# Optimization experiments

Hardware: AMD Instinct MI355X
Metric: run time of the kernel (lower is better)

Reference implementation:

```python
import jax, jax.numpy as jnp
import numpy as np

B, HDIM, H, W = 1, 256, 48, 48
KDIM = 2048
TOP = int(0.1 * KDIM)  # 204, matches int(0.1*self.k)


def _l2norm(v):
    # matches torch F.normalize(dim=1, eps=1e-12)
    return v / jnp.maximum(jnp.linalg.norm(v, axis=1, keepdims=True), 1e-12)


def setup_inputs() -> dict:
    key = jax.random.key(0)
    k1, k2, k3 = jax.random.split(key, 3)
    return {
        "x": jax.random.normal(k1, (B, HDIM, H, W), dtype=jnp.float32),
        "feat_units": jax.random.normal(k2, (KDIM, HDIM), dtype=jnp.float32),
        "label_units": jax.random.normal(k3, (KDIM, 4), dtype=jnp.float32),
    }


def reference(x, feat_units, label_units):
    # update_flag='topk', y=None path of MemoryN2N.forward
    b, c, h, w = x.shape
    xf = x.transpose(0, 2, 3, 1).reshape(-1, c)          # (n, c)
    score = _l2norm(xf) @ _l2norm(feat_units).T           # (n, k) cosine scores
    weight = jax.nn.softmax(score, axis=1)                # (n, k)
    # torch.sort(descending)[1][:, :TOP] == top_k indices (same values)
    _, top_idx = jax.lax.top_k(score, TOP)                # (n, TOP) int32
    sel_wt = jnp.take_along_axis(weight, top_idx, axis=1)  # (n, TOP)
    out_x = jnp.einsum('nk,nkc->nc', sel_wt, feat_units[top_idx])   # (n, c)
    out_y = jnp.einsum('nk,nkc->nc', sel_wt, label_units[top_idx])  # (n, 4)

    def to_img(t, ch):
        return t.reshape(b, h, w, ch).transpose(0, 3, 1, 2)

    out = jnp.concatenate([x, to_img(out_x, c), to_img(out_y, 4)], axis=1)  # (b, 2c+4, h, w)
    return out, score
```

## Files before the change

kernel.cpp:

```cpp
#include <hip/hip_runtime.h>
#include <math.h>

#define N_PIX 2304
#define CDIM  256
#define KDIM  2048
#define TOPK  204

typedef __attribute__((ext_vector_type(8))) short bf16x8;
typedef __attribute__((ext_vector_type(4))) float f32x4;

__device__ __forceinline__ unsigned short f2bf(float f) {
    unsigned u = __float_as_uint(f);
    unsigned r = u + 0x7FFFu + ((u >> 16) & 1u);
    return (unsigned short)(r >> 16);
}
__device__ __forceinline__ float bf2f(unsigned short h) {
    return __uint_as_float((unsigned)h << 16);
}

__device__ __forceinline__ void gload16(const void* g, void* l) {
    __builtin_amdgcn_global_load_lds((const __attribute__((address_space(1))) void*)g,
                                     (__attribute__((address_space(3))) void*)l,
                                     16, 0, 0);
}

__global__ __launch_bounds__(256) void k_prep(const float* __restrict__ x,
                                              const float* __restrict__ feat,
                                              const float* __restrict__ label,
                                              float* __restrict__ out,
                                              unsigned short* __restrict__ xn,
                                              unsigned short* __restrict__ fnorm,
                                              unsigned short* __restrict__ F2T) {
    __shared__ __align__(16) char sm[36864];
    int b = blockIdx.x, t = threadIdx.x;

    if (b < 36) {
        unsigned short* tile = (unsigned short*)sm;
        float* part  = (float*)(sm + 34816);
        float* rnloc = (float*)(sm + 35840);
        int p0 = b * 64;
        #pragma unroll
        for (int i = 0; i < 16; ++i) {
            int g  = i * 256 + t;
            int c  = g >> 4;
            int p4 = g & 15;
            float4 v = *(const float4*)(x + (size_t)c * N_PIX + p0 + p4 * 4);
            *(float4*)(out + (size_t)c * N_PIX + p0 + p4 * 4) = v;
            ushort4 pk;
            pk.x = f2bf(v.x); pk.y = f2bf(v.y); pk.z = f2bf(v.z); pk.w = f2bf(v.w);
            *(ushort4*)&tile[c * 68 + p4 * 4] = pk;
        }
        __syncthreads();
        {
            int pixel = t & 63, q = t >> 6;
            float s = 0.f;
            #pragma unroll
            for (int i = 0; i < 64; ++i) {
                float v = bf2f(tile[(q * 64 + i) * 68 + pixel]);
                s = fmaf(v, v, s);
            }
            part[q * 64 + pixel] = s;
        }
        __syncthreads();
        if (t < 64) {
            float tt = part[t] + part[64 + t] + part[128 + t] + part[192 + t];
            rnloc[t] = 1.0f / fmaxf(sqrtf(tt), 1e-12f);
        }
        __syncthreads();
        {
            int p = t >> 2, cq = t & 3;
            float rn = rnloc[p];
            #pragma unroll
            for (int j = 0; j < 8; ++j) {
                bf16x8 pk;
                #pragma unroll
                for (int jj = 0; jj < 8; ++jj)
                    pk[jj] = (short)f2bf(bf2f(tile[(cq * 64 + j * 8 + jj) * 68 + p]) * rn);
                *(bf16x8*)(xn + (size_t)(p0 + p) * CDIM + cq * 64 + j * 8) = pk;
            }
        }
    } else {
        unsigned short* tile = (unsigned short*)sm;
        int r0 = (b - 36) * 64;
        #pragma unroll
        for (int i = 0; i < 16; ++i) {
            int g  = i * 256 + t;
            int r  = g >> 6;
            int c4 = g & 63;
            float4 v = *(const float4*)(feat + (size_t)(r0 + r) * CDIM + c4 * 4);
            ushort4 pk;
            pk.x = f2bf(v.x); pk.y = f2bf(v.y); pk.z = f2bf(v.z); pk.w = f2bf(v.w);
            *(ushort4*)&tile[r * 264 + c4 * 4] = pk;
        }
        __syncthreads();
        int row = t >> 2, q = t & 3;
        float s = 0.f;
        #pragma unroll
        for (int i = 0; i < 64; ++i) {
            float v = bf2f(tile[row * 264 + q * 64 + i]);
            s = fmaf(v, v, s);
        }
        s += __shfl_xor(s, 1, 64);
        s += __shfl_xor(s, 2, 64);
        float rn = 1.0f / fmaxf(sqrtf(s), 1e-12f);
        #pragma unroll
        for (int j = 0; j < 8; ++j) {
            bf16x8 pk;
            #pragma unroll
            for (int jj = 0; jj < 8; ++jj)
                pk[jj] = (short)f2bf(bf2f(tile[row * 264 + q * 64 + j * 8 + jj]) * rn);
            *(bf16x8*)(fnorm + (size_t)(r0 + row) * CDIM + q * 64 + j * 8) = pk;
        }
        __syncthreads();
        {
            int rp = (t & 31) * 2, cg2 = t >> 5;
            #pragma unroll
            for (int i = 0; i < 32; ++i) {
                int c = i * 8 + cg2;
                unsigned u0 = tile[rp * 264 + c];
                unsigned u1 = tile[(rp + 1) * 264 + c];
                *(unsigned*)(F2T + (size_t)c * KDIM + r0 + rp) = u0 | (u1 << 16);
            }
        }
        {
            int ch = t >> 6, r = t & 63;
            F2T[(size_t)(256 + ch) * KDIM + r0 + r] = f2bf(label[(size_t)(r0 + r) * 4 + ch]);
        }
        #pragma unroll
        for (int i = 0; i < 15; ++i) {
            int idx = t + i * 256;
            int zr = idx >> 6, zc = idx & 63;
            F2T[(size_t)(260 + zr) * KDIM + r0 + zc] = 0;
        }
    }
}

__global__ __launch_bounds__(256) void k_gemm1(const unsigned short* __restrict__ A,
                                               const unsigned short* __restrict__ B,
                                               float* __restrict__ C) {
    __shared__ __align__(16) unsigned short smA[2][128 * 32];
    __shared__ __align__(16) unsigned short smB[2][128 * 32];
    int t = threadIdx.x, l = t & 63, w = t >> 6;
    int m0 = blockIdx.y * 128, n0 = blockIdx.x * 128;
    int wr = w >> 1, wc = w & 1;

    f32x4 acc[4][4] = {};

    #pragma unroll
    for (int r = 0; r < 2; ++r) {
        int row = r * 64 + w * 16 + (l >> 2);
        int ch  = (l & 3) ^ ((row >> 1) & 3);
        gload16(A + (size_t)(m0 + row) * CDIM + ch * 8, &smA[0][(r * 64 + w * 16) * 32]);
        gload16(B + (size_t)(n0 + row) * CDIM + ch * 8, &smB[0][(r * 64 + w * 16) * 32]);
    }
    __syncthreads();

    for (int ks = 0; ks < 8; ++ks) {
        int cur = ks & 1;
        if (ks < 7) {
            int k0 = (ks + 1) * 32;
            #pragma unroll
            for (int r = 0; r < 2; ++r) {
                int row = r * 64 + w * 16 + (l >> 2);
                int ch  = (l & 3) ^ ((row >> 1) & 3);
                gload16(A + (size_t)(m0 + row) * CDIM + k0 + ch * 8, &smA[cur ^ 1][(r * 64 + w * 16) * 32]);
                gload16(B + (size_t)(n0 + row) * CDIM + k0 + ch * 8, &smB[cur ^ 1][(r * 64 + w * 16) * 32]);
            }
        }
        bf16x8 av[4], bv[4];
        #pragma unroll
        for (int mi = 0; mi < 4; ++mi) {
            int R = wr * 64 + mi * 16 + (l & 15);
            av[mi] = *(const bf16x8*)&smA[cur][R * 32 + (((l >> 4) ^ ((R >> 1) & 3)) << 3)];
        }
        #pragma unroll
        for (int ni = 0; ni < 4; ++ni) {
            int R = wc * 64 + ni * 16 + (l & 15);
            bv[ni] = *(const bf16x8*)&smB[cur][R * 32 + (((l >> 4) ^ ((R >> 1) & 3)) << 3)];
        }
        #pragma unroll
        for (int mi = 0; mi < 4; ++mi)
            #pragma unroll
            for (int ni = 0; ni < 4; ++ni)
                acc[mi][ni] = __builtin_amdgcn_mfma_f32_16x16x32_bf16(av[mi], bv[ni], acc[mi][ni], 0, 0, 0);
        __syncthreads();
    }

    #pragma unroll
    for (int mi = 0; mi < 4; ++mi)
        #pragma unroll
        for (int ni = 0; ni < 4; ++ni) {
            int rbase = m0 + wr * 64 + mi * 16 + (l >> 4) * 4;
            int cidx  = n0 + wc * 64 + ni * 16 + (l & 15);
            #pragma unroll
            for (int r = 0; r < 4; ++r)
                C[(size_t)(rbase + r) * KDIM + cidx] = acc[mi][ni][r];
        }
}

__global__ __launch_bounds__(256) void k_select(const float* __restrict__ score,
                                                unsigned short* __restrict__ Wm) {
    int t = threadIdx.x, l = t & 63, w = t >> 6;
    int row = blockIdx.x * 4 + w;
    const float* srow = score + (size_t)row * KDIM;

    float s[32];
    #pragma unroll
    for (int j = 0; j < 8; ++j) {
        float4 v = *(const float4*)(srow + j * 256 + l * 4);
        s[j * 4 + 0] = v.x; s[j * 4 + 1] = v.y; s[j * 4 + 2] = v.z; s[j * 4 + 3] = v.w;
    }

    float d = 0.f;
    #pragma unroll
    for (int j = 0; j < 32; ++j) d += __expf(s[j]);
    #pragma unroll
    for (int off = 32; off; off >>= 1) d += __shfl_xor(d, off, 64);
    float rd = 1.0f / d;

    float lo = -0.25f, hi = 0.75f;
    #pragma unroll 1
    for (int it = 0; it < 18; ++it) {
        float mid = 0.5f * (lo + hi);
        int c = 0;
        #pragma unroll
        for (int j = 0; j < 32; ++j)
            c += (int)__popcll(__ballot(s[j] > mid));
        if (c >= TOPK) lo = mid; else hi = mid;
    }

    #pragma unroll
    for (int j = 0; j < 8; ++j) {
        ushort4 pk;
        pk.x = (s[j*4+0] > lo) ? f2bf(__expf(s[j*4+0]) * rd) : (unsigned short)0;
        pk.y = (s[j*4+1] > lo) ? f2bf(__expf(s[j*4+1]) * rd) : (unsigned short)0;
        pk.z = (s[j*4+2] > lo) ? f2bf(__expf(s[j*4+2]) * rd) : (unsigned short)0;
        pk.w = (s[j*4+3] > lo) ? f2bf(__expf(s[j*4+3]) * rd) : (unsigned short)0;
        *(ushort4*)(Wm + (size_t)row * KDIM + j * 256 + l * 4) = pk;
    }
}

__global__ __launch_bounds__(256) void k_gemm2(const unsigned short* __restrict__ W,
                                               const unsigned short* __restrict__ F2T,
                                               float* __restrict__ out) {
    __shared__ __align__(16) char sm[65536];
    int t = threadIdx.x, l = t & 63, w = t >> 6;
    int m0 = blockIdx.y * 64, n0 = blockIdx.x * 64;
    char* wbase = sm + w * 16384;
    int   kb    = w * 512;

    f32x4 acc[4][4] = {};

    #pragma unroll
    for (int i = 0; i < 4; ++i) {
        int row = i * 16 + (l >> 2);
        int ch  = (l & 3) ^ ((row >> 1) & 3);
        gload16(W   + (size_t)(m0 + row) * KDIM + kb + ch * 8, wbase + i * 1024);
        gload16(F2T + (size_t)(n0 + row) * KDIM + kb + ch * 8, wbase + 8192 + i * 1024);
    }

    for (int ks = 0; ks < 16; ++ks) {
        int cur = ks & 1;
        if (ks < 15) {
            int koff = kb + (ks + 1) * 32;
            #pragma unroll
            for (int i = 0; i < 4; ++i) {
                int row = i * 16 + (l >> 2);
                int ch  = (l & 3) ^ ((row >> 1) & 3);
                gload16(W   + (size_t)(m0 + row) * KDIM + koff + ch * 8, wbase + (cur ^ 1) * 4096 + i * 1024);
                gload16(F2T + (size_t)(n0 + row) * KDIM + koff + ch * 8, wbase + 8192 + (cur ^ 1) * 4096 + i * 1024);
            }
            asm volatile("s_waitcnt vmcnt(8)" ::: "memory");
        } else {
            asm volatile("s_waitcnt vmcnt(0)" ::: "memory");
        }
        bf16x8 av[4], bv[4];
        #pragma unroll
        for (int mi = 0; mi < 4; ++mi) {
            int R = mi * 16 + (l & 15);
            av[mi] = *(const bf16x8*)(wbase + cur * 4096 + R * 64 + (((l >> 4) ^ ((R >> 1) & 3)) << 4));
        }
        #pragma unroll
        for (int ni = 0; ni < 4; ++ni) {
            int R = ni * 16 + (l & 15);
            bv[ni] = *(const bf16x8*)(wbase + 8192 + cur * 4096 + R * 64 + (((l >> 4) ^ ((R >> 1) & 3)) << 4));
        }
        #pragma unroll
        for (int mi = 0; mi < 4; ++mi)
            #pragma unroll
            for (int ni = 0; ni < 4; ++ni)
                acc[mi][ni] = __builtin_amdgcn_mfma_f32_16x16x32_bf16(av[mi], bv[ni], acc[mi][ni], 0, 0, 0);
    }

    __syncthreads();
    float* tl = (float*)sm;
    if (w >= 2) {
        float* dst = tl + (w - 2) * 64 * 65;
        #pragma unroll
        for (int mi = 0; mi < 4; ++mi)
            #pragma unroll
            for (int ni = 0; ni < 4; ++ni) {
                int rr = mi * 16 + (l >> 4) * 4;
                int cc = ni * 16 + (l & 15);
                #pragma unroll
                for (int r = 0; r < 4; ++r)
                    dst[(rr + r) * 65 + cc] = acc[mi][ni][r];
            }
    }
    __syncthreads();
    if (w < 2) {
        float* dst = tl + w * 64 * 65;
        #pragma unroll
        for (int mi = 0; mi < 4; ++mi)
            #pragma unroll
            for (int ni = 0; ni < 4; ++ni) {
                int rr = mi * 16 + (l >> 4) * 4;
                int cc = ni * 16 + (l & 15);
                #pragma unroll
                for (int r = 0; r < 4; ++r)
                    dst[(rr + r) * 65 + cc] += acc[mi][ni][r];
            }
    }
    __syncthreads();
    int pl = t & 63, cg2 = t >> 6;
    #pragma unroll
    for (int i = 0; i < 16; ++i) {
        int cc = cg2 * 16 + i;
        int c_out = n0 + cc;
        int orow;
        if (c_out < 256) orow = 256 + c_out;
        else if (c_out < 260) orow = 512 + (c_out - 256);
        else continue;
        out[(size_t)orow * N_PIX + m0 + pl] = tl[pl * 65 + cc] + tl[64 * 65 + pl * 65 + cc];
    }
}

extern "C" void kernel_launch(void* const* d_in, const int* in_sizes, int n_in,
                              void* d_out, int out_size, void* d_ws, size_t ws_size,
                              hipStream_t stream) {
    const float* x     = (const float*)d_in[0];
    const float* feat  = (const float*)d_in[1];
    const float* label = (const float*)d_in[2];
    float* out   = (float*)d_out;
    float* score = out + 516 * N_PIX;

    char* ws = (char*)d_ws;
    unsigned short* xn    = (unsigned short*)(ws);
    unsigned short* fnorm = (unsigned short*)(ws + 1179648);
    unsigned short* F2T   = (unsigned short*)(ws + 2228224);
    unsigned short* Wm    = (unsigned short*)(ws + 3538944);

    k_prep  <<<68,           256, 0, stream>>>(x, feat, label, out, xn, fnorm, F2T);
    k_gemm1 <<<dim3(16, 18), 256, 0, stream>>>(xn, fnorm, score);
    k_select<<<576,          256, 0, stream>>>(score, Wm);
    k_gemm2 <<<dim3(5, 36),  256, 0, stream>>>(Wm, F2T, out);
}
```

Measured before the change: 52.37 us.

## Shrink prep and gemm1 tiles for more blocks; threshold on exp values in select

The prep kernel now handles 16 pixels or 16 feature rows per block instead of 64, which quadruples the grid to 272 blocks and reworks the per-thread reduction and transpose mappings. gemm1 uses 64-row M tiles, doubling its grid to 576 blocks so more of the GPU's compute units are occupied. The select kernel computes exp once, reuses it for the softmax denominator, the threshold bisection (bounds moved into exp space) and the output, which removes the repeated exp calls. In exchange, operand reuse per block drops in gemm1 and more blocks and launches add overhead.

```diff
diff --git a/kernel.cpp b/kernel.cpp
--- a/kernel.cpp
+++ b/kernel.cpp
@@ -31,59 +31,62 @@
                                               unsigned short* __restrict__ xn,
                                               unsigned short* __restrict__ fnorm,
                                               unsigned short* __restrict__ F2T) {
-    __shared__ __align__(16) char sm[36864];
+    __shared__ __align__(16) char sm[12288];
     int b = blockIdx.x, t = threadIdx.x;
 
-    if (b < 36) {
+    if (b < 144) {
         unsigned short* tile = (unsigned short*)sm;
-        float* part  = (float*)(sm + 34816);
-        float* rnloc = (float*)(sm + 35840);
-        int p0 = b * 64;
-        #pragma unroll
-        for (int i = 0; i < 16; ++i) {
+        float* part  = (float*)(sm + 10240);
+        float* rnloc = (float*)(sm + 11264);
+        int p0 = b * 16;
+        #pragma unroll
+        for (int i = 0; i < 4; ++i) {
             int g  = i * 256 + t;
-            int c  = g >> 4;
-            int p4 = g & 15;
+            int c  = g >> 2;
+            int p4 = g & 3;
             float4 v = *(const float4*)(x + (size_t)c * N_PIX + p0 + p4 * 4);
             *(float4*)(out + (size_t)c * N_PIX + p0 + p4 * 4) = v;
             ushort4 pk;
             pk.x = f2bf(v.x); pk.y = f2bf(v.y); pk.z = f2bf(v.z); pk.w = f2bf(v.w);
-            *(ushort4*)&tile[c * 68 + p4 * 4] = pk;
+            *(ushort4*)&tile[c * 20 + p4 * 4] = pk;
         }
         __syncthreads();
         {
-            int pixel = t & 63, q = t >> 6;
+            int px = t & 15, cg = t >> 4;
             float s = 0.f;
             #pragma unroll
-            for (int i = 0; i < 64; ++i) {
-                float v = bf2f(tile[(q * 64 + i) * 68 + pixel]);
+            for (int i = 0; i < 16; ++i) {
+                float v = bf2f(tile[(cg * 16 + i) * 20 + px]);
                 s = fmaf(v, v, s);
             }
-            part[q * 64 + pixel] = s;
-        }
-        __syncthreads();
-        if (t < 64) {
-            float tt = part[t] + part[64 + t] + part[128 + t] + part[192 + t];
+            part[cg * 16 + px] = s;
+        }
+        __syncthreads();
+        if (t < 16) {
+            float tt = 0.f;
+            #pragma unroll
+            for (int cg = 0; cg < 16; ++cg) tt += part[cg * 16 + t];
             rnloc[t] = 1.0f / fmaxf(sqrtf(tt), 1e-12f);
         }
         __syncthreads();
         {
-            int p = t >> 2, cq = t & 3;
-            float rn = rnloc[p];
-            #pragma unroll
-            for (int j = 0; j < 8; ++j) {
+            int px = t >> 4;
+            float rn = rnloc[px];
+            #pragma unroll
+            for (int ji = 0; ji < 2; ++ji) {
+                int j = (t & 15) + ji * 16;
                 bf16x8 pk;
                 #pragma unroll
                 for (int jj = 0; jj < 8; ++jj)
-                    pk[jj] = (short)f2bf(bf2f(tile[(cq * 64 + j * 8 + jj) * 68 + p]) * rn);
-                *(bf16x8*)(xn + (size_t)(p0 + p) * CDIM + cq * 64 + j * 8) = pk;
+                    pk[jj] = (short)f2bf(bf2f(tile[(j * 8 + jj) * 20 + px]) * rn);
+                *(bf16x8*)(xn + (size_t)(p0 + px) * CDIM + j * 8) = pk;
             }
         }
     } else {
         unsigned short* tile = (unsigned short*)sm;
-        int r0 = (b - 36) * 64;
-        #pragma unroll
-        for (int i = 0; i < 16; ++i) {
+        int r0 = (b - 144) * 16;
+        #pragma unroll
+        for (int i = 0; i < 4; ++i) {
             int g  = i * 256 + t;
             int r  = g >> 6;
             int c4 = g & 63;
@@ -93,44 +96,50 @@
             *(ushort4*)&tile[r * 264 + c4 * 4] = pk;
         }
         __syncthreads();
-        int row = t >> 2, q = t & 3;
+        int row = t >> 4, q = t & 15;
         float s = 0.f;
         #pragma unroll
-        for (int i = 0; i < 64; ++i) {
-            float v = bf2f(tile[row * 264 + q * 64 + i]);
+        for (int i = 0; i < 16; ++i) {
+            float v = bf2f(tile[row * 264 + q * 16 + i]);
             s = fmaf(v, v, s);
         }
         s += __shfl_xor(s, 1, 64);
         s += __shfl_xor(s, 2, 64);
+        s += __shfl_xor(s, 4, 64);
+        s += __shfl_xor(s, 8, 64);
         float rn = 1.0f / fmaxf(sqrtf(s), 1e-12f);
         #pragma unroll
-        for (int j = 0; j < 8; ++j) {
+        for (int ji = 0; ji < 2; ++ji) {
+            int j = q + ji * 16;
             bf16x8 pk;
             #pragma unroll
             for (int jj = 0; jj < 8; ++jj)
-                pk[jj] = (short)f2bf(bf2f(tile[row * 264 + q * 64 + j * 8 + jj]) * rn);
-            *(bf16x8*)(fnorm + (size_t)(r0 + row) * CDIM + q * 64 + j * 8) = pk;
+                pk[jj] = (short)f2bf(bf2f(tile[row * 264 + j * 8 + jj]) * rn);
+            *(bf16x8*)(fnorm + (size_t)(r0 + row) * CDIM + j * 8) = pk;
         }
         __syncthreads();
         {
-            int rp = (t & 31) * 2, cg2 = t >> 5;
-            #pragma unroll
-            for (int i = 0; i < 32; ++i) {
-                int c = i * 8 + cg2;
-                unsigned u0 = tile[rp * 264 + c];
-                unsigned u1 = tile[(rp + 1) * 264 + c];
-                *(unsigned*)(F2T + (size_t)c * KDIM + r0 + rp) = u0 | (u1 << 16);
-            }
-        }
-        {
-            int ch = t >> 6, r = t & 63;
+            int c = t;
+            #pragma unroll
+            for (int h = 0; h < 2; ++h) {
+                bf16x8 pk;
+                #pragma unroll
+                for (int r = 0; r < 8; ++r)
+                    pk[r] = (short)tile[(h * 8 + r) * 264 + c];
+                *(bf16x8*)(F2T + (size_t)c * KDIM + r0 + h * 8) = pk;
+            }
+        }
+        if (t < 64) {
+            int ch = t >> 4, r = t & 15;
             F2T[(size_t)(256 + ch) * KDIM + r0 + r] = f2bf(label[(size_t)(r0 + r) * 4 + ch]);
         }
         #pragma unroll
-        for (int i = 0; i < 15; ++i) {
-            int idx = t + i * 256;
-            int zr = idx >> 6, zc = idx & 63;
-            F2T[(size_t)(260 + zr) * KDIM + r0 + zc] = 0;
+        for (int i = 0; i < 4; ++i) {
+            int idx = i * 256 + t;
+            if (idx < 960) {
+                int zr = idx >> 4, zc = idx & 15;
+                F2T[(size_t)(260 + zr) * KDIM + r0 + zc] = 0;
+            }
         }
     }
 }
@@ -138,20 +147,24 @@
 __global__ __launch_bounds__(256) void k_gemm1(const unsigned short* __restrict__ A,
                                                const unsigned short* __restrict__ B,
                                                float* __restrict__ C) {
-    __shared__ __align__(16) unsigned short smA[2][128 * 32];
+    __shared__ __align__(16) unsigned short smA[2][64 * 32];
     __shared__ __align__(16) unsigned short smB[2][128 * 32];
     int t = threadIdx.x, l = t & 63, w = t >> 6;
-    int m0 = blockIdx.y * 128, n0 = blockIdx.x * 128;
+    int m0 = blockIdx.y * 64, n0 = blockIdx.x * 128;
     int wr = w >> 1, wc = w & 1;
 
-    f32x4 acc[4][4] = {};
-
-    #pragma unroll
-    for (int r = 0; r < 2; ++r) {
-        int row = r * 64 + w * 16 + (l >> 2);
-        int ch  = (l & 3) ^ ((row >> 1) & 3);
-        gload16(A + (size_t)(m0 + row) * CDIM + ch * 8, &smA[0][(r * 64 + w * 16) * 32]);
-        gload16(B + (size_t)(n0 + row) * CDIM + ch * 8, &smB[0][(r * 64 + w * 16) * 32]);
+    f32x4 acc[2][4] = {};
+
+    {
+        int rowA = w * 16 + (l >> 2);
+        int chA  = (l & 3) ^ ((rowA >> 1) & 3);
+        gload16(A + (size_t)(m0 + rowA) * CDIM + chA * 8, &smA[0][(w * 16) * 32]);
+        #pragma unroll
+        for (int i = 0; i < 2; ++i) {
+            int rowB = i * 64 + w * 16 + (l >> 2);
+            int chB  = (l & 3) ^ ((rowB >> 1) & 3);
+            gload16(B + (size_t)(n0 + rowB) * CDIM + chB * 8, &smB[0][(i * 64 + w * 16) * 32]);
+        }
     }
     __syncthreads();
 
@@ -159,18 +172,20 @@
         int cur = ks & 1;
         if (ks < 7) {
             int k0 = (ks + 1) * 32;
-            #pragma unroll
-            for (int r = 0; r < 2; ++r) {
-                int row = r * 64 + w * 16 + (l >> 2);
-                int ch  = (l & 3) ^ ((row >> 1) & 3);
-                gload16(A + (size_t)(m0 + row) * CDIM + k0 + ch * 8, &smA[cur ^ 1][(r * 64 + w * 16) * 32]);
-                gload16(B + (size_t)(n0 + row) * CDIM + k0 + ch * 8, &smB[cur ^ 1][(r * 64 + w * 16) * 32]);
-            }
-        }
-        bf16x8 av[4], bv[4];
-        #pragma unroll
-        for (int mi = 0; mi < 4; ++mi) {
-            int R = wr * 64 + mi * 16 + (l & 15);
+            int rowA = w * 16 + (l >> 2);
+            int chA  = (l & 3) ^ ((rowA >> 1) & 3);
+            gload16(A + (size_t)(m0 + rowA) * CDIM + k0 + chA * 8, &smA[cur ^ 1][(w * 16) * 32]);
+            #pragma unroll
+            for (int i = 0; i < 2; ++i) {
+                int rowB = i * 64 + w * 16 + (l >> 2);
+                int chB  = (l & 3) ^ ((rowB >> 1) & 3);
+                gload16(B + (size_t)(n0 + rowB) * CDIM + k0 + chB * 8, &smB[cur ^ 1][(i * 64 + w * 16) * 32]);
+            }
+        }
+        bf16x8 av[2], bv[4];
+        #pragma unroll
+        for (int mi = 0; mi < 2; ++mi) {
+            int R = wr * 32 + mi * 16 + (l & 15);
             av[mi] = *(const bf16x8*)&smA[cur][R * 32 + (((l >> 4) ^ ((R >> 1) & 3)) << 3)];
         }
         #pragma unroll
@@ -179,7 +194,7 @@
             bv[ni] = *(const bf16x8*)&smB[cur][R * 32 + (((l >> 4) ^ ((R >> 1) & 3)) << 3)];
         }
         #pragma unroll
-        for (int mi = 0; mi < 4; ++mi)
+        for (int mi = 0; mi < 2; ++mi)
             #pragma unroll
             for (int ni = 0; ni < 4; ++ni)
                 acc[mi][ni] = __builtin_amdgcn_mfma_f32_16x16x32_bf16(av[mi], bv[ni], acc[mi][ni], 0, 0, 0);
@@ -187,10 +202,10 @@
     }
 
     #pragma unroll
-    for (int mi = 0; mi < 4; ++mi)
+    for (int mi = 0; mi < 2; ++mi)
         #pragma unroll
         for (int ni = 0; ni < 4; ++ni) {
-            int rbase = m0 + wr * 64 + mi * 16 + (l >> 4) * 4;
+            int rbase = m0 + wr * 32 + mi * 16 + (l >> 4) * 4;
             int cidx  = n0 + wc * 64 + ni * 16 + (l & 15);
             #pragma unroll
             for (int r = 0; r < 4; ++r)
@@ -204,38 +219,37 @@
     int row = blockIdx.x * 4 + w;
     const float* srow = score + (size_t)row * KDIM;
 
-    float s[32];
+    float e[32];
+    float d = 0.f;
     #pragma unroll
     for (int j = 0; j < 8; ++j) {
         float4 v = *(const float4*)(srow + j * 256 + l * 4);
-        s[j * 4 + 0] = v.x; s[j * 4 + 1] = v.y; s[j * 4 + 2] = v.z; s[j * 4 + 3] = v.w;
-    }
-
-    float d = 0.f;
-    #pragma unroll
-    for (int j = 0; j < 32; ++j) d += __expf(s[j]);
+        e[j * 4 + 0] = __expf(v.x); e[j * 4 + 1] = __expf(v.y);
+        e[j * 4 + 2] = __expf(v.z); e[j * 4 + 3] = __expf(v.w);
+        d += e[j*4+0] + e[j*4+1] + e[j*4+2] + e[j*4+3];
+    }
     #pragma unroll
     for (int off = 32; off; off >>= 1) d += __shfl_xor(d, off, 64);
     float rd = 1.0f / d;
 
-    float lo = -0.25f, hi = 0.75f;
+    float lo = 0.36f, hi = 2.72f;
     #pragma unroll 1
     for (int it = 0; it < 18; ++it) {
         float mid = 0.5f * (lo + hi);
         int c = 0;
         #pragma unroll
         for (int j = 0; j < 32; ++j)
-            c += (int)__popcll(__ballot(s[j] > mid));
+            c += (int)__popcll(__ballot(e[j] > mid));
         if (c >= TOPK) lo = mid; else hi = mid;
     }
 
     #pragma unroll
     for (int j = 0; j < 8; ++j) {
         ushort4 pk;
-        pk.x = (s[j*4+0] > lo) ? f2bf(__expf(s[j*4+0]) * rd) : (unsigned short)0;
-        pk.y = (s[j*4+1] > lo) ? f2bf(__expf(s[j*4+1]) * rd) : (unsigned short)0;
-        pk.z = (s[j*4+2] > lo) ? f2bf(__expf(s[j*4+2]) * rd) : (unsigned short)0;
-        pk.w = (s[j*4+3] > lo) ? f2bf(__expf(s[j*4+3]) * rd) : (unsigned short)0;
+        pk.x = (e[j*4+0] > lo) ? f2bf(e[j*4+0] * rd) : (unsigned short)0;
+        pk.y = (e[j*4+1] > lo) ? f2bf(e[j*4+1] * rd) : (unsigned short)0;
+        pk.z = (e[j*4+2] > lo) ? f2bf(e[j*4+2] * rd) : (unsigned short)0;
+        pk.w = (e[j*4+3] > lo) ? f2bf(e[j*4+3] * rd) : (unsigned short)0;
         *(ushort4*)(Wm + (size_t)row * KDIM + j * 256 + l * 4) = pk;
     }
 }
@@ -350,8 +364,8 @@
     unsigned short* F2T   = (unsigned short*)(ws + 2228224);
     unsigned short* Wm    = (unsigned short*)(ws + 3538944);
 
-    k_prep  <<<68,           256, 0, stream>>>(x, feat, label, out, xn, fnorm, F2T);
-    k_gemm1 <<<dim3(16, 18), 256, 0, stream>>>(xn, fnorm, score);
+    k_prep  <<<272,          256, 0, stream>>>(x, feat, label, out, xn, fnorm, F2T);
+    k_gemm1 <<<dim3(16, 36), 256, 0, stream>>>(xn, fnorm, score);
     k_select<<<576,          256, 0, stream>>>(score, Wm);
     k_gemm2 <<<dim3(5, 36),  256, 0, stream>>>(Wm, F2T, out);
 }
```

After: 49.69 us, median of 2. 5.1% less time.
